# Kernel tuning notes

Hardware: AMD Instinct MI355X
Metric: run time of the kernel (lower is better)

Reference implementation:

```python
import jax, jax.numpy as jnp
import numpy as np

# ---- static model dims (from init_kwargs) ----
M = 128          # latent_seq_length
Mp1 = M + 1
K = 2 * Mp1      # HMM states (m,g): m in 0..M, g in {0: match, 1: insert}; k = m + (M+1)*g
D = 21           # alphabet_length
ZD = 64          # z_dim
B = 64           # batch size
L = 256          # obs_seq_length
P = Mp1 * 3 * 2  # flattened indel-parameter count (M+1, 3, 2)
NEG = -1e32      # -1/epsilon (pyro Profile epsilon=1e-32) -> forbidden transitions


def _cell_factors(n0, g, mp, gp):
    """Indel log-prob factors (param indices (m,j,s)) for a transition into state (mp,gp)
    when the next undecided ancestral slot is n0 and source type is j=g.
    j: 0=from match, 1=from insert, 2=after deletion. s: 0=no indel, 1=indel.
    Returns (insert_factors, delete_factors) or None if the transition is forbidden."""
    if mp < n0:
        return None
    rs, us = [], []
    if mp == n0:
        if gp == 0:
            rs.append((n0, g, 0)); us.append((n0, g, 0))
        else:
            rs.append((n0, g, 1))
    else:
        rs.append((n0, g, 0)); us.append((n0, g, 1))
        for mm in range(n0 + 1, mp):
            rs.append((mm, 2, 0)); us.append((mm, 2, 1))
        if gp == 0:
            rs.append((mp, 2, 0)); us.append((mp, 2, 0))
        else:
            rs.append((mp, 2, 1))
    return rs, us


def _build_tables():
    k_of = lambda m, g: m + Mp1 * g
    p_of = lambda m, j, s: (m * 3 + j) * 2 + s
    # initial-distribution transfer (dense, small): virtual source (m,g)=(-1,0) -> n0=0
    r0 = np.zeros((P, K), np.float32)
    u0 = np.zeros((P, K), np.float32)
    null0 = np.zeros((K,), np.float32)
    for mp in range(Mp1):
        for gp in range(2):
            f = _cell_factors(0, 0, mp, gp)
            kp = k_of(mp, gp)
            if f is None:
                null0[kp] = 1.0
            else:
                for t in f[0]:
                    r0[p_of(*t), kp] += 1.0
                for t in f[1]:
                    u0[p_of(*t), kp] += 1.0
    # transition-matrix transfer: sparse (param_idx, cell_idx) scatter-add lists
    r_par, r_cell, u_par, u_cell = [], [], [], []
    null = np.zeros((K, K), np.float32)
    for m in range(Mp1):
        for g in range(2):
            n0, k = m + 1 - g, k_of(m, g)
            for mp in range(Mp1):
                for gp in range(2):
                    kp = k_of(mp, gp)
                    f = _cell_factors(n0, g, mp, gp)
                    if f is None:
                        null[k, kp] = 1.0
                    else:
                        cell = k * K + kp
                        for t in f[0]:
                            r_par.append(p_of(*t)); r_cell.append(cell)
                        for t in f[1]:
                            u_par.append(p_of(*t)); u_cell.append(cell)
    return (jnp.asarray(r0), jnp.asarray(u0), jnp.asarray(null0), jnp.asarray(null),
            jnp.asarray(np.asarray(r_par, np.int32)), jnp.asarray(np.asarray(r_cell, np.int32)),
            jnp.asarray(np.asarray(u_par, np.int32)), jnp.asarray(np.asarray(u_cell, np.int32)))


R0, U0, NULL0, NULL, R_PAR, R_CELL, U_PAR, U_CELL = _build_tables()


def setup_inputs() -> dict:
    key = jax.random.key(0)
    ks = jax.random.split(key, 8)
    # variable-length one-hot sequences; missing steps are all-zero rows (pyro convention)
    tokens = jax.random.randint(ks[0], (B, L), 0, D)
    lengths = jax.random.randint(ks[1], (B,), L // 2, L + 1)
    mask = jnp.arange(L)[None, :] < lengths[:, None]
    data = jax.nn.one_hot(tokens, D, dtype=jnp.float32) * mask[:, :, None]
    z = jax.random.normal(ks[2], (B, ZD), jnp.float32)
    out_dim = 2 * Mp1 * D
    dec_W = jax.random.normal(ks[3], (out_dim, ZD), jnp.float32) / np.sqrt(ZD).astype(np.float32)
    dec_b = jax.random.normal(ks[4], (out_dim,), jnp.float32) * 0.01
    indel_prior = jnp.array([10.0, 0.0], jnp.float32)  # [strength, 0]
    insert = indel_prior + jax.random.normal(ks[5], (Mp1, 3, 2), jnp.float32)
    delete = indel_prior + jax.random.normal(ks[6], (Mp1, 3, 2), jnp.float32)
    inverse_temp = 1.0 + 0.1 * jax.random.normal(ks[7], (1,), jnp.float32)
    return {"data": data, "z": z, "dec_W": dec_W, "dec_b": dec_b,
            "insert": insert, "delete": delete, "inverse_temp": inverse_temp}


def reference(data, z, dec_W, dec_b, insert, delete, inverse_temp):
    # ---- Decoder + temperature-sharpened emission logits (FactorMuE.model) ----
    latent = (z @ dec_W.T + dec_b).reshape(-1, 2, Mp1, D)        # (B, 2, M+1, D)
    it = jax.nn.softplus(inverse_temp[0])
    anc = latent[:, 0] * it
    anc = anc - jax.nn.logsumexp(anc, axis=-1, keepdims=True)    # ancestor_seq_logits
    insq = latent[:, 1] * it
    insq = insq - jax.nn.logsumexp(insq, axis=-1, keepdims=True)  # insert_seq_logits
    ilog = insert - jax.nn.logsumexp(insert, axis=-1, keepdims=True)
    dlog = delete - jax.nn.logsumexp(delete, axis=-1, keepdims=True)
    # ---- Profile state arranger: profile-HMM -> dense HMM logits ----
    pi, pd = ilog.reshape(-1), dlog.reshape(-1)                  # (P,)
    a0 = pd @ U0 + pi @ R0 + NEG * NULL0                         # (K,) initial logits
    a = (jnp.zeros((K * K,), pi.dtype)
         .at[U_CELL].add(pd[U_PAR])
         .at[R_CELL].add(pi[R_PAR])).reshape(K, K) + NEG * NULL  # (K, K) transition logits
    e = jnp.concatenate([anc, insq], axis=1)                     # (B, K, D), k = m + (M+1)*g
    # ---- VariableLengthDiscreteHMM (MissingDataDiscreteHMM) log_prob ----
    a0 = a0 - jax.nn.logsumexp(a0)
    a = a - jax.nn.logsumexp(a, axis=-1, keepdims=True)
    e = e - jax.nn.logsumexp(e, axis=-1, keepdims=True)
    vl = jnp.einsum('bld,bkd->lbk', data, e)                     # (L, B, K); zero rows -> 0 (missing)
    alpha = a0 + vl[0]                                           # (B, K)

    def step(alpha, v):
        alpha = jax.nn.logsumexp(alpha[:, :, None] + a[None], axis=1) + v
        return alpha, None

    alpha, _ = jax.lax.scan(step, alpha, vl[1:])
    return jax.nn.logsumexp(alpha, axis=-1)                      # (B,) log-likelihood per sequence
```

## Files before the change

### kernel.cpp

```cpp
#include <hip/hip_runtime.h>
#include <math.h>

#define MP1 129
#define KK  258
#define DD  21
#define ZDIM 64
#define BB  64
#define LL  256
#define EROW 260
#define ETOK 22

#define OFF_TOK  366080
#define OFF_COEF 382464
#define C_UU   0
#define C_DXM  258
#define C_DXI  516
#define C_WM   774
#define C_WI   903
#define C_DMID 1032
#define C_PI0  1160

#define EMIS_BLKS 65
#define TOK_BLKS  1366

typedef float f32x2 __attribute__((ext_vector_type(2)));

template <int CTRL, int RM, int BM>
__device__ __forceinline__ float updpp(float old, float src) {
    return __int_as_float(__builtin_amdgcn_update_dpp(
        __float_as_int(old), __float_as_int(src), CTRL, RM, BM, false));
}
__device__ __forceinline__ float readlane_f(float v, int lane) {
    return __int_as_float(__builtin_amdgcn_readlane(__float_as_int(v), lane));
}
__device__ __forceinline__ float wave_sum_to63(float s) {
    s += updpp<0x111, 0xf, 0xf>(0.f, s);
    s += updpp<0x112, 0xf, 0xf>(0.f, s);
    s += updpp<0x114, 0xf, 0xf>(0.f, s);
    s += updpp<0x118, 0xf, 0xf>(0.f, s);
    s += updpp<0x142, 0xa, 0xf>(0.f, s);
    s += updpp<0x143, 0xc, 0xf>(0.f, s);
    return s;
}

__global__ __launch_bounds__(256) void k_setup(const float* __restrict__ z,
                                               const float* __restrict__ W,
                                               const float* __restrict__ bias,
                                               const float* __restrict__ invt,
                                               const float* __restrict__ data,
                                               const float* __restrict__ ins,
                                               const float* __restrict__ del,
                                               float* __restrict__ E,
                                               int* __restrict__ tokout,
                                               float* __restrict__ coef) {
    __shared__ float il[774], dl[774], Smid[129], Qs[130];
    int bid = blockIdx.x;
    int tid = threadIdx.x;

    if (bid >= 1 && bid <= EMIS_BLKS) {
        int b  = tid & 63;
        int rr = __builtin_amdgcn_readfirstlane((bid - 1) * 4 + (tid >> 6));
        if (rr >= KK) return;
        float it = log1pf(expf(invt[0]));
        float4 zr[16];
        const float4* zp = (const float4*)(z + (size_t)b * ZDIM);
        #pragma unroll
        for (int j = 0; j < 16; ++j) zr[j] = zp[j];
        const float* wb = W + (size_t)rr * DD * ZDIM;
        const float* bp = bias + rr * DD;
        float acc[DD];
        #pragma unroll
        for (int d = 0; d < DD; ++d) {
            const float4* wp = (const float4*)(wb + d * ZDIM);
            float a = bp[d];
            #pragma unroll
            for (int j = 0; j < 16; ++j) {
                float4 w4 = wp[j];
                a += zr[j].x * w4.x + zr[j].y * w4.y + zr[j].z * w4.z + zr[j].w * w4.w;
            }
            acc[d] = a * it;
        }
        float mx = acc[0];
        #pragma unroll
        for (int d = 1; d < DD; ++d) mx = fmaxf(mx, acc[d]);
        float s = 0.f;
        #pragma unroll
        for (int d = 0; d < DD; ++d) { acc[d] = expf(acc[d] - mx); s += acc[d]; }
        float inv = 1.0f / s;
        float* Eb = E + (size_t)b * ETOK * EROW;
        int col = (rr < MP1) ? rr : (rr + 1);
        #pragma unroll
        for (int d = 0; d < DD; ++d) Eb[d * EROW + col] = acc[d] * inv;
        Eb[DD * EROW + col] = 1.0f;
        return;
    }
    if (bid > EMIS_BLKS) {
        int wid  = (bid - 1 - EMIS_BLKS) * 4 + (tid >> 6);
        int lane = tid & 63;
        int r3   = lane / 21;
        int d    = lane - r3 * 21;
        int row  = wid * 3 + r3;
        float v = 0.f;
        if (r3 < 3 && row < BB * LL) v = data[(size_t)row * DD + d];
        unsigned long long m = __ballot(v > 0.5f);
        if (r3 < 3 && d == 0 && row < BB * LL) {
            unsigned long long slice = (m >> (21 * r3)) & 0x1FFFFFULL;
            tokout[row] = slice ? (int)__builtin_ctzll(slice) : DD;
        }
        return;
    }
    int t = tid;
    for (int p = t; p < 387; p += 256) {
        float x0 = ins[2 * p], x1 = ins[2 * p + 1];
        float mx = fmaxf(x0, x1);
        float ls = mx + logf(expf(x0 - mx) + expf(x1 - mx));
        il[2 * p] = x0 - ls; il[2 * p + 1] = x1 - ls;
        float y0 = del[2 * p], y1 = del[2 * p + 1];
        float my = fmaxf(y0, y1);
        float lt = my + logf(expf(y0 - my) + expf(y1 - my));
        dl[2 * p] = y0 - lt; dl[2 * p + 1] = y1 - lt;
    }
    __syncthreads();
    if (t < 64) {
        int mmA = 1 + 2 * t, mmB = 2 + 2 * t;
        float xA = il[(mmA * 3 + 2) * 2 + 0] + dl[(mmA * 3 + 2) * 2 + 1];
        float xB = il[(mmB * 3 + 2) * 2 + 0] + dl[(mmB * 3 + 2) * 2 + 1];
        float sc = xA + xB;
        #pragma unroll
        for (int off = 1; off < 64; off <<= 1) {
            float vv = __shfl_up(sc, off);
            if (t >= off) sc += vv;
        }
        Smid[mmB] = sc;
        Smid[mmA] = sc - xB;
        if (t == 0) Smid[0] = 0.f;
    }
    __syncthreads();
    if (t < 64) {
        int mpA = 128 - 2 * t, mpB = 127 - 2 * t;
        float aM_ = il[(mpA * 3 + 2) * 2 + 0] + dl[(mpA * 3 + 2) * 2 + 0];
        float aI_ = il[(mpA * 3 + 2) * 2 + 1];
        float mA = fmaxf(aM_, aI_);
        float pA = Smid[mpA - 1] + mA + logf(expf(aM_ - mA) + expf(aI_ - mA));
        float bM_ = il[(mpB * 3 + 2) * 2 + 0] + dl[(mpB * 3 + 2) * 2 + 0];
        float bI_ = il[(mpB * 3 + 2) * 2 + 1];
        float mB = fmaxf(bM_, bI_);
        float pB = Smid[mpB - 1] + mB + logf(expf(bM_ - mB) + expf(bI_ - mB));
        float cm = fmaxf(pA, pB);
        float cs = expf(pA - cm) + expf(pB - cm);
        #pragma unroll
        for (int off = 1; off < 64; off <<= 1) {
            float om = __shfl_up(cm, off);
            float os = __shfl_up(cs, off);
            if (t >= off) {
                float M = fmaxf(cm, om);
                cs = cs * expf(cm - M) + os * expf(om - M);
                cm = M;
            }
        }
        Qs[mpB] = cm + logf(cs);
        float em = __shfl_up(cm, 1), es = __shfl_up(cs, 1);
        if (t == 0) Qs[128] = pA;
        else {
            float M = fmaxf(em, pA);
            Qs[mpA] = M + logf(es * expf(em - M) + expf(pA - M));
        }
        if (t == 0) Qs[129] = -1e30f;
    }
    __syncthreads();
    float* uu  = coef + C_UU;
    float* dxM = coef + C_DXM;
    float* dxI = coef + C_DXI;
    float* wM  = coef + C_WM;
    float* wI  = coef + C_WI;
    float* dmd = coef + C_DMID;
    float* pi0 = coef + C_PI0;
    for (int k = t; k < KK; k += 256) {
        if (k == 128) { uu[k] = 0.f; dxM[k] = 0.f; dxI[k] = 0.f; continue; }
        int g  = (k < MP1) ? 0 : 1;
        int n0 = g ? (k - MP1) : (k + 1);
        float i0 = il[(n0 * 3 + g) * 2 + 0], i1 = il[(n0 * 3 + g) * 2 + 1];
        float e0 = dl[(n0 * 3 + g) * 2 + 0], e1 = dl[(n0 * 3 + g) * 2 + 1];
        float diagM = i0 + e0;
        float diagI = i1;
        float src   = i0 + e1;
        float tail  = src - Smid[n0] + Qs[n0 + 1];
        float M3 = fmaxf(fmaxf(diagM, diagI), tail);
        float ssum = expf(diagM - M3) + expf(diagI - M3) + expf(tail - M3);
        float lse = M3 + logf(ssum);
        uu[k]  = expf(src - lse);
        dxM[k] = expf(diagM - lse);
        dxI[k] = expf(diagI - lse);
    }
    for (int mp = t; mp < MP1; mp += 256) {
        wM[mp] = expf(il[(mp * 3 + 2) * 2 + 0] + dl[(mp * 3 + 2) * 2 + 0]);
        wI[mp] = expf(il[(mp * 3 + 2) * 2 + 1]);
    }
    for (int tt = t; tt < 128; tt += 256)
        dmd[tt] = (tt == 0) ? 1.f : expf(il[(tt * 3 + 2) * 2 + 0] + dl[(tt * 3 + 2) * 2 + 1]);
    __syncthreads();
    {
        float i00 = il[0], i01 = il[1], d00 = dl[0], d01 = dl[1];
        float a00 = i00 + d00, a0129 = i01;
        float tail0 = i00 + d01 + Qs[1];
        float M3 = fmaxf(fmaxf(a00, a0129), tail0);
        float lse0 = M3 + logf(expf(a00 - M3) + expf(a0129 - M3) + expf(tail0 - M3));
        for (int kp = t; kp < KK; kp += 256) {
            int gp = (kp >= MP1);
            int mp = gp ? (kp - MP1) : kp;
            float v;
            if (mp == 0) v = gp ? a0129 : a00;
            else v = i00 + d01 + Smid[mp - 1] +
                     (gp ? il[(mp * 3 + 2) * 2 + 1]
                         : il[(mp * 3 + 2) * 2 + 0] + dl[(mp * 3 + 2) * 2 + 0]);
            pi0[kp] = expf(v - lse0);
        }
    }
}

__global__ __launch_bounds__(64) void k_fwd(const float* __restrict__ Eg,
                                            const int* __restrict__ tokg,
                                            const float* __restrict__ coef,
                                            float* __restrict__ out) {
    const float* uu  = coef + C_UU;
    const float* dxM = coef + C_DXM;
    const float* dxI = coef + C_DXI;
    const float* wMg = coef + C_WM;
    const float* wIg = coef + C_WI;
    const float* dmd = coef + C_DMID;
    const float* pi0 = coef + C_PI0;
    __shared__ float Eo[ETOK * EROW];
    __shared__ float ETL[ETOK * 64 * 4];
    __shared__ float E2L[ETOK * 2];
    int lane = threadIdx.x;
    int b = blockIdx.x;
    const float4* s4 = (const float4*)(Eg + (size_t)b * ETOK * EROW);
    float4* d4 = (float4*)Eo;
    for (int i = lane; i < ETOK * EROW / 4; i += 64) d4[i] = s4[i];
    int4 tkv = ((const int4*)(tokg + b * LL))[lane];
    __syncthreads();
    for (int d = 0; d < ETOK; ++d) {
        const float* r = Eo + d * EROW;
        f32x2 em = *(const f32x2*)(r + 2 * lane);
        f32x2 ei = *(const f32x2*)(r + 130 + 2 * lane);
        float4 v4 = {em.x, em.y, ei.x, ei.y};
        *(float4*)(ETL + (d * 64 + lane) * 4) = v4;
    }
    if (lane < ETOK) {
        E2L[lane * 2 + 0] = Eo[lane * EROW + 128];
        E2L[lane * 2 + 1] = Eo[lane * EROW + 258];
    }
    __syncthreads();

    int m0 = 2 * lane, m1 = 2 * lane + 1;
    bool L0 = (lane == 0), L63 = (lane == 63);
    float f63 = L63 ? 1.f : 0.f;
    float cM0 = L0 ? 0.f : uu[m0 - 1];
    float cI0 = uu[129 + m0];
    float cM1 = uu[m0];
    float cI1 = uu[129 + m1];
    float d0 = dmd[m0], d1v = dmd[m1];
    float Apair = d0 * d1v;
    f32x2 wMp  = {wMg[m0], wMg[m1]};
    f32x2 wIp  = {wIg[m0], wIg[m1]};
    f32x2 xMAp = {L0 ? 0.f : dxM[m0 - 1], dxM[m0]};
    f32x2 xIAp = {L0 ? 0.f : dxI[m0 - 1], dxI[m0]};
    f32x2 xMBp = {dxM[129 + m0], dxM[129 + m1]};
    f32x2 xIBp = {dxI[129 + m0], dxI[129 + m1]};
    f32x2 w2p  = {L63 ? wMg[128] : 0.f, L63 ? wIg[128] : 0.f};
    f32x2 xA2p = {L63 ? dxM[127] : 0.f, L63 ? dxI[127] : 0.f};
    f32x2 xB2p = {L63 ? dxM[257] : 0.f, L63 ? dxI[257] : 0.f};
    f32x2 f63p = {f63, f63};

    float A0 = Apair;
    float A1 = A0 * updpp<0x111, 0xf, 0xf>(1.f, A0);
    float A2 = A1 * updpp<0x112, 0xf, 0xf>(1.f, A1);
    float A3 = A2 * updpp<0x114, 0xf, 0xf>(1.f, A2);
    float A4 = A3 * updpp<0x118, 0xf, 0xf>(1.f, A3);
    float A5 = A4 * updpp<0x142, 0xa, 0xf>(1.f, A4);

    int tok0 = __builtin_amdgcn_readlane(tkv.x, 0);
    float4 q0 = *(const float4*)(ETL + (tok0 * 64 + lane) * 4);
    f32x2 e20 = *(const f32x2*)(E2L + tok0 * 2);
    f32x2 aM = {pi0[m0] * q0.x, pi0[m1] * q0.y};
    f32x2 aI = {pi0[129 + m0] * q0.z, pi0[129 + m1] * q0.w};
    f32x2 a2 = {f63 * pi0[128] * e20.x, f63 * pi0[257] * e20.y};

    int etot = 0;
    f32x2 part = (aM + aI) + a2;

    float4 q1, q2, q3, q4;
    f32x2 e21, e22, e23, e24;
#define LOADR(QN, EN, TN)                                                    \
    { int tn_ = (TN);                                                        \
      QN = *(const float4*)(ETL + (tn_ * 64 + lane) * 4);                    \
      EN = *(const f32x2*)(E2L + tn_ * 2); }
    LOADR(q1, e21, __builtin_amdgcn_readlane(tkv.y, 0));
    LOADR(q2, e22, __builtin_amdgcn_readlane(tkv.z, 0));
    LOADR(q3, e23, __builtin_amdgcn_readlane(tkv.w, 0));
    LOADR(q4, e24, __builtin_amdgcn_readlane(tkv.x, 1));

#define STEP_BODY(RES, Qr, E2r)                                              \
    {                                                                        \
        f32x2 EMv = {Qr.x, Qr.y};                                            \
        f32x2 EIv = {Qr.z, Qr.w};                                            \
        f32x2 E2v = E2r;                                                     \
        if (RES) {                                                           \
            float s_ = wave_sum_to63(part.x + part.y);                       \
            float stot = readlane_f(s_, 63);                                 \
            int sb = __float_as_int(stot) & 0x7f800000;                      \
            etot += (sb >> 23);                                              \
            float invs = __int_as_float(0x7f000000 - sb);                    \
            f32x2 iv = {invs, invs};                                         \
            EMv *= iv; EIv *= iv; E2v *= iv;                                 \
        }                                                                    \
        float aMp  = updpp<0x138, 0xf, 0xf>(0.f, aM.y);        \
        float u128 = readlane_f(a2.x, 63);                                   \
        float r0 = fmaf(aMp, cM0, aI.x * cI0);                               \
        float r1 = fmaf(aM.x, cM1, aI.y * cI1);                              \
        float B = fmaf(d1v, r0, r1);                                         \
        B = fmaf(A0, updpp<0x111, 0xf, 0xf>(0.f, B), B);                     \
        B = fmaf(A1, updpp<0x112, 0xf, 0xf>(0.f, B), B);                     \
        B = fmaf(A2, updpp<0x114, 0xf, 0xf>(0.f, B), B);                     \
        B = fmaf(A3, updpp<0x118, 0xf, 0xf>(0.f, B), B);                     \
        B = fmaf(A4, updpp<0x142, 0xa, 0xf>(0.f, B), B);                     \
        B = fmaf(A5, updpp<0x143, 0xc, 0xf>(0.f, B), B);                     \
        float G0 = updpp<0x138, 0xf, 0xf>(0.f, B);                           \
        float G1 = fmaf(d0, G0, r0);                                         \
        f32x2 Gp   = {G0, G1};                                               \
        f32x2 aMs  = {aMp, aM.x};                                            \
        f32x2 u2   = {u128, u128};                                           \
        f32x2 G2p  = {B, B};                                                 \
        f32x2 aM1s = {aM.y, aM.y};                                           \
        f32x2 aI2s = {a2.y, a2.y};                                           \
        f32x2 mM = wMp * Gp + (xMAp * aMs + (xMBp * aI + u2));               \
        f32x2 mI = wIp * Gp + (xIAp * aMs + (xIBp * aI + u2));               \
        f32x2 m2 = w2p * G2p + (xA2p * aM1s + (xB2p * aI2s + u2));           \
        aM = mM * EMv;                                                       \
        aI = mI * EIv;                                                       \
        a2 = m2 * E2v * f63p;                                                \
        part = (aM + aI) + a2;                                               \
    }

    for (int it = 0; it < 63; ++it) {
        STEP_BODY(1, q1, e21);
        LOADR(q1, e21, __builtin_amdgcn_readlane(tkv.y, it + 1));
        STEP_BODY(0, q2, e22);
        LOADR(q2, e22, __builtin_amdgcn_readlane(tkv.z, it + 1));
        STEP_BODY(0, q3, e23);
        LOADR(q3, e23, __builtin_amdgcn_readlane(tkv.w, it + 1));
        STEP_BODY(0, q4, e24);
        int it2 = (it + 2 < 64) ? (it + 2) : 63;
        LOADR(q4, e24, __builtin_amdgcn_readlane(tkv.x, it2));
    }
    STEP_BODY(1, q1, e21);
    STEP_BODY(0, q2, e22);
    STEP_BODY(0, q3, e23);
#undef STEP_BODY
#undef LOADR

    float s = wave_sum_to63(part.x + part.y);
    if (lane == 63)
        out[b] = (float)(etot - 64 * 127) * 0.6931471805599453f + logf(s);
}

extern "C" void kernel_launch(void* const* d_in, const int* in_sizes, int n_in,
                              void* d_out, int out_size, void* d_ws, size_t ws_size,
                              hipStream_t stream) {
    const float* data  = (const float*)d_in[0];
    const float* z     = (const float*)d_in[1];
    const float* dec_W = (const float*)d_in[2];
    const float* dec_b = (const float*)d_in[3];
    const float* ins   = (const float*)d_in[4];
    const float* del   = (const float*)d_in[5];
    const float* invt  = (const float*)d_in[6];
    float* out = (float*)d_out;

    float* ws   = (float*)d_ws;
    float* E    = ws;
    int*   tok  = (int*)(ws + OFF_TOK);
    float* coef = ws + OFF_COEF;

    k_setup<<<1 + EMIS_BLKS + TOK_BLKS, 256, 0, stream>>>(z, dec_W, dec_b, invt,
                                                          data, ins, del, E, tok, coef);
    k_fwd<<<BB, 64, 0, stream>>>(E, tok, coef, out);
}
```

Before: 59.39 us.

## Truncate scan prefix levels when decay products underflow; restructure emission GEMV

The forward scan now checks with a wave ballot whether the cumulative deletion-product coefficients A2/A3 are all zero. It then dispatches to a specialised copy of the scan loop that drops the unneeded DPP prefix-scan levels. The per-step partial-sum update is computed only on the steps that precede a rescale. In the setup kernel, the emission matvec is reorganised to stream z in chunks with explicit FMAs instead of holding all of z in registers, and launch bounds add min-blocks 1. The truncation is exact only when the products really are zero in float, and it triples the scan code size.

```diff
diff --git a/kernel.cpp b/kernel.cpp
--- a/kernel.cpp
+++ b/kernel.cpp
@@ -43,16 +43,16 @@
     return s;
 }
 
-__global__ __launch_bounds__(256) void k_setup(const float* __restrict__ z,
-                                               const float* __restrict__ W,
-                                               const float* __restrict__ bias,
-                                               const float* __restrict__ invt,
-                                               const float* __restrict__ data,
-                                               const float* __restrict__ ins,
-                                               const float* __restrict__ del,
-                                               float* __restrict__ E,
-                                               int* __restrict__ tokout,
-                                               float* __restrict__ coef) {
+__global__ __launch_bounds__(256, 1) void k_setup(const float* __restrict__ z,
+                                                  const float* __restrict__ W,
+                                                  const float* __restrict__ bias,
+                                                  const float* __restrict__ invt,
+                                                  const float* __restrict__ data,
+                                                  const float* __restrict__ ins,
+                                                  const float* __restrict__ del,
+                                                  float* __restrict__ E,
+                                                  int* __restrict__ tokout,
+                                                  float* __restrict__ coef) {
     __shared__ float il[774], dl[774], Smid[129], Qs[130];
     int bid = blockIdx.x;
     int tid = threadIdx.x;
@@ -62,27 +62,35 @@
         int rr = __builtin_amdgcn_readfirstlane((bid - 1) * 4 + (tid >> 6));
         if (rr >= KK) return;
         float it = log1pf(expf(invt[0]));
-        float4 zr[16];
-        const float4* zp = (const float4*)(z + (size_t)b * ZDIM);
-        #pragma unroll
-        for (int j = 0; j < 16; ++j) zr[j] = zp[j];
         const float* wb = W + (size_t)rr * DD * ZDIM;
         const float* bp = bias + rr * DD;
         float acc[DD];
         #pragma unroll
-        for (int d = 0; d < DD; ++d) {
-            const float4* wp = (const float4*)(wb + d * ZDIM);
-            float a = bp[d];
+        for (int d = 0; d < DD; ++d) acc[d] = bp[d];
+        const float4* zp = (const float4*)(z + (size_t)b * ZDIM);
+        #pragma unroll
+        for (int c = 0; c < 4; ++c) {
+            float4 za = zp[4 * c + 0], zb = zp[4 * c + 1];
+            float4 zc = zp[4 * c + 2], zd = zp[4 * c + 3];
             #pragma unroll
-            for (int j = 0; j < 16; ++j) {
-                float4 w4 = wp[j];
-                a += zr[j].x * w4.x + zr[j].y * w4.y + zr[j].z * w4.z + zr[j].w * w4.w;
+            for (int d = 0; d < DD; ++d) {
+                const float4* wp = (const float4*)(wb + (size_t)d * ZDIM + 16 * c);
+                float4 wa = wp[0], wv = wp[1], wc = wp[2], wd = wp[3];
+                float a = acc[d];
+                a = fmaf(za.x, wa.x, a); a = fmaf(za.y, wa.y, a);
+                a = fmaf(za.z, wa.z, a); a = fmaf(za.w, wa.w, a);
+                a = fmaf(zb.x, wv.x, a); a = fmaf(zb.y, wv.y, a);
+                a = fmaf(zb.z, wv.z, a); a = fmaf(zb.w, wv.w, a);
+                a = fmaf(zc.x, wc.x, a); a = fmaf(zc.y, wc.y, a);
+                a = fmaf(zc.z, wc.z, a); a = fmaf(zc.w, wc.w, a);
+                a = fmaf(zd.x, wd.x, a); a = fmaf(zd.y, wd.y, a);
+                a = fmaf(zd.z, wd.z, a); a = fmaf(zd.w, wd.w, a);
+                acc[d] = a;
             }
-            acc[d] = a * it;
-        }
-        float mx = acc[0];
-        #pragma unroll
-        for (int d = 1; d < DD; ++d) mx = fmaxf(mx, acc[d]);
+        }
+        float mx = acc[0] * it;
+        #pragma unroll
+        for (int d = 0; d < DD; ++d) { acc[d] *= it; mx = fmaxf(mx, acc[d]); }
         float s = 0.f;
         #pragma unroll
         for (int d = 0; d < DD; ++d) { acc[d] = expf(acc[d] - mx); s += acc[d]; }
@@ -278,6 +286,9 @@
     float A3 = A2 * updpp<0x114, 0xf, 0xf>(1.f, A2);
     float A4 = A3 * updpp<0x118, 0xf, 0xf>(1.f, A3);
     float A5 = A4 * updpp<0x142, 0xa, 0xf>(1.f, A4);
+    unsigned long long bb2 = __ballot(A2 != 0.f);
+    unsigned long long bb3 = __ballot(A3 != 0.f);
+    int nlev = (bb2 == 0ULL) ? 2 : ((bb3 == 0ULL) ? 3 : 6);
 
     int tok0 = __builtin_amdgcn_readlane(tkv.x, 0);
     float4 q0 = *(const float4*)(ETL + (tok0 * 64 + lane) * 4);
@@ -300,7 +311,7 @@
     LOADR(q3, e23, __builtin_amdgcn_readlane(tkv.w, 0));
     LOADR(q4, e24, __builtin_amdgcn_readlane(tkv.x, 1));
 
-#define STEP_BODY(RES, Qr, E2r)                                              \
+#define STEP_BODY(RES, PART, NLEV, Qr, E2r)                                  \
     {                                                                        \
         f32x2 EMv = {Qr.x, Qr.y};                                            \
         f32x2 EIv = {Qr.z, Qr.w};                                            \
@@ -321,10 +332,12 @@
         float B = fmaf(d1v, r0, r1);                                         \
         B = fmaf(A0, updpp<0x111, 0xf, 0xf>(0.f, B), B);                     \
         B = fmaf(A1, updpp<0x112, 0xf, 0xf>(0.f, B), B);                     \
-        B = fmaf(A2, updpp<0x114, 0xf, 0xf>(0.f, B), B);                     \
-        B = fmaf(A3, updpp<0x118, 0xf, 0xf>(0.f, B), B);                     \
-        B = fmaf(A4, updpp<0x142, 0xa, 0xf>(0.f, B), B);                     \
-        B = fmaf(A5, updpp<0x143, 0xc, 0xf>(0.f, B), B);                     \
+        if (NLEV > 2) B = fmaf(A2, updpp<0x114, 0xf, 0xf>(0.f, B), B);       \
+        if (NLEV > 3) B = fmaf(A3, updpp<0x118, 0xf, 0xf>(0.f, B), B);       \
+        if (NLEV > 4) {                                                      \
+            B = fmaf(A4, updpp<0x142, 0xa, 0xf>(0.f, B), B);                 \
+            B = fmaf(A5, updpp<0x143, 0xc, 0xf>(0.f, B), B);                 \
+        }                                                                    \
         float G0 = updpp<0x138, 0xf, 0xf>(0.f, B);                           \
         float G1 = fmaf(d0, G0, r0);                                         \
         f32x2 Gp   = {G0, G1};                                               \
@@ -339,23 +352,29 @@
         aM = mM * EMv;                                                       \
         aI = mI * EIv;                                                       \
         a2 = m2 * E2v * f63p;                                                \
-        part = (aM + aI) + a2;                                               \
-    }
-
-    for (int it = 0; it < 63; ++it) {
-        STEP_BODY(1, q1, e21);
-        LOADR(q1, e21, __builtin_amdgcn_readlane(tkv.y, it + 1));
-        STEP_BODY(0, q2, e22);
-        LOADR(q2, e22, __builtin_amdgcn_readlane(tkv.z, it + 1));
-        STEP_BODY(0, q3, e23);
-        LOADR(q3, e23, __builtin_amdgcn_readlane(tkv.w, it + 1));
-        STEP_BODY(0, q4, e24);
-        int it2 = (it + 2 < 64) ? (it + 2) : 63;
-        LOADR(q4, e24, __builtin_amdgcn_readlane(tkv.x, it2));
-    }
-    STEP_BODY(1, q1, e21);
-    STEP_BODY(0, q2, e22);
-    STEP_BODY(0, q3, e23);
+        if (PART) part = (aM + aI) + a2;                                     \
+    }
+
+#define RUN_SCAN(NLEV)                                                       \
+    for (int it = 0; it < 63; ++it) {                                        \
+        STEP_BODY(1, 0, NLEV, q1, e21);                                      \
+        LOADR(q1, e21, __builtin_amdgcn_readlane(tkv.y, it + 1));            \
+        STEP_BODY(0, 0, NLEV, q2, e22);                                      \
+        LOADR(q2, e22, __builtin_amdgcn_readlane(tkv.z, it + 1));            \
+        STEP_BODY(0, 0, NLEV, q3, e23);                                      \
+        LOADR(q3, e23, __builtin_amdgcn_readlane(tkv.w, it + 1));            \
+        STEP_BODY(0, 1, NLEV, q4, e24);                                      \
+        int it2 = (it + 2 < 64) ? (it + 2) : 63;                             \
+        LOADR(q4, e24, __builtin_amdgcn_readlane(tkv.x, it2));               \
+    }                                                                        \
+    STEP_BODY(1, 0, NLEV, q1, e21);                                          \
+    STEP_BODY(0, 0, NLEV, q2, e22);                                          \
+    STEP_BODY(0, 1, NLEV, q3, e23);
+
+    if (nlev == 2)      { RUN_SCAN(2) }
+    else if (nlev == 3) { RUN_SCAN(3) }
+    else                { RUN_SCAN(6) }
+#undef RUN_SCAN
 #undef STEP_BODY
 #undef LOADR
 
```

Measured after the change: 54.65 us. -8.0%, faster.
